# Performance work log

Measured on AMD Instinct MI355X. Metric: run time of the kernel, lower is better.

The kernel has to match this reference:

```python
import math
import jax, jax.numpy as jnp
import numpy as np

RATIO = 0.5
N_CHANNELS = 64
B = 64
N_PER = 8192  # nodes per batch element (equal counts for a regular reference)
D_POS = 3


def setup_inputs() -> dict:
    key = jax.random.key(0)
    k1, k2, k3 = jax.random.split(key, 3)
    N = B * N_PER
    positions = jax.random.normal(k1, (N, D_POS), dtype=jnp.float32)
    weights = jax.random.normal(k2, (N, N_CHANNELS), dtype=jnp.float32)
    w = jax.random.normal(k3, (N_CHANNELS,), dtype=jnp.float32)  # SelectTopK learnable vector
    batch = jnp.full((B,), N_PER, dtype=jnp.int32)  # per-batch-element node counts
    return {"positions": positions, "weights": weights, "w": w, "batch": batch}


def reference(positions, weights, w, batch):
    # SelectTopK: score = tanh((x @ w) / ||w||), then per-batch top-ceil(ratio*n) selection.
    n_b = batch.shape[0]
    n_per = positions.shape[0] // n_b
    k = int(math.ceil(RATIO * n_per))

    score = jnp.tanh((weights @ w) / jnp.linalg.norm(w))          # [N]
    top_vals, top_idx = jax.lax.top_k(score.reshape(n_b, n_per), k)  # [B,k] each

    # global node indices of selected nodes (descending score within each batch element)
    node_index = (top_idx + jnp.arange(n_b, dtype=top_idx.dtype)[:, None] * n_per).reshape(-1)  # [B*k]

    pos_sel = positions[node_index]                               # [B*k, D_POS]
    w_sel = weights[node_index] * top_vals.reshape(-1)[:, None]   # [B*k, C] gated by score
    # histc recount: each batch element keeps exactly k nodes
    new_batch = jnp.full((n_b,), k, dtype=jnp.int32)
    return pos_sel, w_sel, new_batch
```

## Files before the change

kernel.cpp:

```cpp
#include <hip/hip_runtime.h>
#include <math.h>

#define C 64
#define DPOS 3
#define NPER 8192
#define KK 4096

typedef unsigned long long ull;

__device__ __forceinline__ ull make_key(float s, unsigned idx) {
    unsigned u = __float_as_uint(s);
    unsigned o = (u >> 31) ? ~u : (u | 0x80000000u);
    unsigned d = ~o;
    return ((ull)d << 32) | (ull)idx;
}
__device__ __forceinline__ float key_score(ull key) {
    unsigned o = ~(unsigned)(key >> 32);
    unsigned u = (o >> 31) ? (o & 0x7FFFFFFFu) : ~o;
    return __uint_as_float(u);
}

__global__ __launch_bounds__(256) void score_kernel(const float* __restrict__ weights,
                                                    const float* __restrict__ w,
                                                    ull* __restrict__ keys, int n) {
    int wid = (blockIdx.x * blockDim.x + threadIdx.x) >> 6;
    int lane = threadIdx.x & 63;
    int c4 = lane & 15, sub = lane >> 4;
    const float4* wv4 = (const float4*)w;
    float nrm = 0.f;
    #pragma unroll
    for (int i = 0; i < 16; ++i) {
        float4 t = wv4[i];
        nrm += t.x * t.x + t.y * t.y + t.z * t.z + t.w * t.w;
    }
    float nw = sqrtf(nrm);
    float4 wv = wv4[c4];
    #pragma unroll
    for (int it = 0; it < 4; ++it) {
        int r = wid * 16 + it * 4 + sub;
        float4 x = ((const float4*)weights)[(size_t)r * 16 + c4];
        float acc = x.x * wv.x + x.y * wv.y + x.z * wv.z + x.w * wv.w;
        #pragma unroll
        for (int off = 8; off >= 1; off >>= 1) acc += __shfl_xor(acc, off, 16);
        if (c4 == 0 && r < n)
            keys[r] = make_key(tanhf(acc / nw), (unsigned)(r & (NPER - 1)));
    }
}

#define CH 2048
#define CTH 1024
__global__ __launch_bounds__(CTH) void sort_chunk(ull* __restrict__ keys) {
    __shared__ ull lds[CH];
    const int tid = threadIdx.x;
    ull* bk = keys + (size_t)blockIdx.x * CH;
    #pragma unroll
    for (int s = 0; s < CH / CTH; ++s) lds[tid + s * CTH] = bk[tid + s * CTH];
    for (unsigned k = 2; k <= CH; k <<= 1) {
        for (unsigned j = k >> 1; j > 0; j >>= 1) {
            __syncthreads();
            #pragma unroll
            for (int s = 0; s < CH / CTH; ++s) {
                unsigned i = tid + s * CTH;
                unsigned ixj = i ^ j;
                if (ixj > i) {
                    ull a = lds[i], b = lds[ixj];
                    bool up = ((i & k) == 0);
                    if ((a > b) == up) { lds[i] = b; lds[ixj] = a; }
                }
            }
        }
    }
    __syncthreads();
    #pragma unroll
    for (int s = 0; s < CH / CTH; ++s) bk[tid + s * CTH] = lds[tid + s * CTH];
}

#define MT 256
#define MTILE 1024
__global__ __launch_bounds__(MT) void merge_tiled(const ull* __restrict__ src,
                                                  ull* __restrict__ dst,
                                                  int L, int tilesPerPair, int outStride) {
    __shared__ ull in[MTILE];
    __shared__ ull ob[MTILE];
    __shared__ int sAB[2];
    int tile = blockIdx.x;
    int pair = tile / tilesPerPair;
    int o0 = (tile - pair * tilesPerPair) * MTILE;
    const ull* A = src + (size_t)pair * (2 * L);
    const ull* B = A + L;
    ull* D = dst + (size_t)pair * outStride;
    int tid = threadIdx.x;
    if (tid < 2) {
        int o = o0 + tid * MTILE;
        int lo = o - L; if (lo < 0) lo = 0;
        int hi = o < L ? o : L;
        while (lo < hi) {
            int m = (lo + hi) >> 1;
            if (A[m] < B[o - 1 - m]) lo = m + 1; else hi = m;
        }
        sAB[tid] = lo;
    }
    __syncthreads();
    int aLo = sAB[0], aHi = sAB[1];
    int na = aHi - aLo;
    int bLo = o0 - aLo;
    int nb2 = MTILE - na;
    for (int i = tid; i < na; i += MT) in[i] = A[aLo + i];
    for (int i = tid; i < nb2; i += MT) in[na + i] = B[bLo + i];
    __syncthreads();
    int o = tid * 4;
    int lo = o - nb2; if (lo < 0) lo = 0;
    int hi = o < na ? o : na;
    while (lo < hi) {
        int m = (lo + hi) >> 1;
        if (in[m] < in[na + o - 1 - m]) lo = m + 1; else hi = m;
    }
    int a = lo, b = o - lo;
    #pragma unroll
    for (int t = 0; t < 4; ++t) {
        bool fromA = (b >= nb2) || (a < na && in[a] < in[na + b]);
        ob[o + t] = fromA ? in[a++] : in[na + b++];
    }
    __syncthreads();
    for (int i = tid; i < MTILE; i += MT) D[o0 + i] = ob[i];
}

__global__ __launch_bounds__(1024) void sort_full(ull* __restrict__ keys) {
    __shared__ ull lds[NPER];
    const unsigned tid = threadIdx.x;
    ull* bk = keys + (size_t)blockIdx.x * NPER;
    #pragma unroll
    for (int s = 0; s < NPER / 1024; ++s) lds[tid + s * 1024] = bk[tid + s * 1024];
    for (unsigned k = 2; k <= NPER; k <<= 1) {
        for (unsigned j = k >> 1; j > 0; j >>= 1) {
            __syncthreads();
            #pragma unroll
            for (int s = 0; s < NPER / 1024; ++s) {
                unsigned i = tid + s * 1024;
                unsigned ixj = i ^ j;
                if (ixj > i) {
                    ull a = lds[i], b = lds[ixj];
                    bool up = ((i & k) == 0);
                    if ((a > b) == up) { lds[i] = b; lds[ixj] = a; }
                }
            }
        }
    }
    __syncthreads();
    #pragma unroll
    for (int s = 0; s < NPER / 1024; ++s) bk[tid + s * 1024] = lds[tid + s * 1024];
}

__global__ __launch_bounds__(256) void gather_kernel(const float* __restrict__ positions,
                                                     const float* __restrict__ weights,
                                                     const ull* __restrict__ keys,
                                                     float* __restrict__ out_pos,
                                                     float* __restrict__ out_w,
                                                     float* __restrict__ out_batch,
                                                     int rows, int nb, int kstr) {
    int gid = blockIdx.x * blockDim.x + threadIdx.x;
    if (gid < nb) out_batch[gid] = (float)KK;
    int lane = gid & 63;
    int sub = lane >> 4, c4 = lane & 15;
    int r = (gid >> 6) * 4 + sub;
    if (r >= rows) return;
    int b = r >> 12;
    int j = r & (KK - 1);
    ull key = keys[(size_t)b * kstr + j];
    unsigned idx = (unsigned)key;
    size_t node = ((size_t)b << 13) + idx;
    float s = key_score(key);
    float4 x = ((const float4*)weights)[node * 16 + c4];
    float4 y; y.x = x.x * s; y.y = x.y * s; y.z = x.z * s; y.w = x.w * s;
    ((float4*)out_w)[(size_t)r * 16 + c4] = y;
    if (c4 < DPOS)
        out_pos[(size_t)r * DPOS + c4] = positions[node * DPOS + c4];
}

extern "C" void kernel_launch(void* const* d_in, const int* in_sizes, int n_in,
                              void* d_out, int out_size, void* d_ws, size_t ws_size,
                              hipStream_t stream) {
    const float* positions = (const float*)d_in[0];
    const float* weights   = (const float*)d_in[1];
    const float* w         = (const float*)d_in[2];

    int n  = in_sizes[1] / C;
    int nb = in_sizes[3];
    int rows = nb * KK;

    ull* bufA = (ull*)d_ws;
    ull* bufB = bufA + n;
    bool have_dbuf = ws_size >= (size_t)n * 2 * sizeof(ull);

    score_kernel<<<n / 64, 256, 0, stream>>>(weights, w, bufA, n);

    const ull* sorted_keys;
    int kstr;
    if (have_dbuf) {
        sort_chunk<<<n / CH, CTH, 0, stream>>>(bufA);
        merge_tiled<<<n / MTILE, MT, 0, stream>>>(bufA, bufB, 2048, 4, 4096);
        merge_tiled<<<(nb * KK) / MTILE, MT, 0, stream>>>(bufB, bufA, 4096, 4, KK);
        sorted_keys = bufA; kstr = KK;
    } else {
        sort_full<<<nb, 1024, 0, stream>>>(bufA);
        sorted_keys = bufA; kstr = NPER;
    }

    long long gthreads = (long long)(rows / 4) * 64;
    gather_kernel<<<(int)((gthreads + 255) / 256), 256, 0, stream>>>(
        positions, weights, sorted_keys, (float*)d_out,
        (float*)d_out + (size_t)rows * DPOS,
        (float*)d_out + (size_t)rows * (DPOS + C),
        rows, nb, kstr);
}
```

Baseline: 280.5 us.

## Fuse scoring into chunk sort and merge each batch in one LDS kernel

The score computation now writes keys straight into shared memory inside the 2048-element bitonic chunk sort, so the key buffer no longer makes a separate global round trip. The two tiled global merge passes are replaced by one kernel per batch element. That kernel loads all 8192 sorted keys into LDS, runs the 2048→4096 merge in shared memory, and writes only the top 4096 from the final merge. This removes two launches and several global key read/write passes. The cost is much lower parallelism: the score pass now runs on only 256 large blocks, and the merge on one block per batch. That may hurt memory-level parallelism when streaming the weights.

```diff
diff --git a/kernel.cpp b/kernel.cpp
--- a/kernel.cpp
+++ b/kernel.cpp
@@ -20,12 +20,13 @@
     return __uint_as_float(u);
 }
 
-__global__ __launch_bounds__(256) void score_kernel(const float* __restrict__ weights,
-                                                    const float* __restrict__ w,
-                                                    ull* __restrict__ keys, int n) {
-    int wid = (blockIdx.x * blockDim.x + threadIdx.x) >> 6;
-    int lane = threadIdx.x & 63;
-    int c4 = lane & 15, sub = lane >> 4;
+#define CH 2048
+#define CTH 1024
+__global__ __launch_bounds__(CTH) void score_sort(const float* __restrict__ weights,
+                                                  const float* __restrict__ w,
+                                                  ull* __restrict__ keys) {
+    __shared__ ull lds[CH];
+    const int tid = threadIdx.x;
     const float4* wv4 = (const float4*)w;
     float nrm = 0.f;
     #pragma unroll
@@ -34,27 +35,20 @@
         nrm += t.x * t.x + t.y * t.y + t.z * t.z + t.w * t.w;
     }
     float nw = sqrtf(nrm);
+    const int r16 = tid >> 4;
+    const int c4  = tid & 15;
     float4 wv = wv4[c4];
-    #pragma unroll
-    for (int it = 0; it < 4; ++it) {
-        int r = wid * 16 + it * 4 + sub;
-        float4 x = ((const float4*)weights)[(size_t)r * 16 + c4];
+    const size_t base = (size_t)blockIdx.x * CH;
+    #pragma unroll 4
+    for (int it = 0; it < CH / 64; ++it) {
+        int rl = it * 64 + r16;
+        float4 x = ((const float4*)weights)[(base + rl) * 16 + c4];
         float acc = x.x * wv.x + x.y * wv.y + x.z * wv.z + x.w * wv.w;
         #pragma unroll
         for (int off = 8; off >= 1; off >>= 1) acc += __shfl_xor(acc, off, 16);
-        if (c4 == 0 && r < n)
-            keys[r] = make_key(tanhf(acc / nw), (unsigned)(r & (NPER - 1)));
-    }
-}
-
-#define CH 2048
-#define CTH 1024
-__global__ __launch_bounds__(CTH) void sort_chunk(ull* __restrict__ keys) {
-    __shared__ ull lds[CH];
-    const int tid = threadIdx.x;
-    ull* bk = keys + (size_t)blockIdx.x * CH;
-    #pragma unroll
-    for (int s = 0; s < CH / CTH; ++s) lds[tid + s * CTH] = bk[tid + s * CTH];
+        if (c4 == 0)
+            lds[rl] = make_key(tanhf(acc / nw), (unsigned)((base + rl) & (NPER - 1)));
+    }
     for (unsigned k = 2; k <= CH; k <<= 1) {
         for (unsigned j = k >> 1; j > 0; j >>= 1) {
             __syncthreads();
@@ -72,57 +66,58 @@
     }
     __syncthreads();
     #pragma unroll
-    for (int s = 0; s < CH / CTH; ++s) bk[tid + s * CTH] = lds[tid + s * CTH];
-}
-
-#define MT 256
-#define MTILE 1024
-__global__ __launch_bounds__(MT) void merge_tiled(const ull* __restrict__ src,
-                                                  ull* __restrict__ dst,
-                                                  int L, int tilesPerPair, int outStride) {
-    __shared__ ull in[MTILE];
-    __shared__ ull ob[MTILE];
-    __shared__ int sAB[2];
-    int tile = blockIdx.x;
-    int pair = tile / tilesPerPair;
-    int o0 = (tile - pair * tilesPerPair) * MTILE;
-    const ull* A = src + (size_t)pair * (2 * L);
-    const ull* B = A + L;
-    ull* D = dst + (size_t)pair * outStride;
-    int tid = threadIdx.x;
-    if (tid < 2) {
-        int o = o0 + tid * MTILE;
-        int lo = o - L; if (lo < 0) lo = 0;
-        int hi = o < L ? o : L;
+    for (int s = 0; s < CH / CTH; ++s) keys[base + tid + s * CTH] = lds[tid + s * CTH];
+}
+
+__global__ __launch_bounds__(1024) void merge_batch(const ull* __restrict__ src,
+                                                    ull* __restrict__ dst) {
+    __shared__ ull ld[NPER];
+    const int tid = threadIdx.x;
+    const ull* bk = src + (size_t)blockIdx.x * NPER;
+    #pragma unroll
+    for (int s = 0; s < NPER / 1024; ++s) ld[tid + s * 1024] = bk[tid + s * 1024];
+    __syncthreads();
+    ull r[8];
+    {
+        int p = tid >> 9;
+        int o = (tid & 511) * 8;
+        const ull* A = ld + p * 4096;
+        const ull* B = A + 2048;
+        int lo = o - 2048; if (lo < 0) lo = 0;
+        int hi = o < 2048 ? o : 2048;
         while (lo < hi) {
             int m = (lo + hi) >> 1;
             if (A[m] < B[o - 1 - m]) lo = m + 1; else hi = m;
         }
-        sAB[tid] = lo;
-    }
-    __syncthreads();
-    int aLo = sAB[0], aHi = sAB[1];
-    int na = aHi - aLo;
-    int bLo = o0 - aLo;
-    int nb2 = MTILE - na;
-    for (int i = tid; i < na; i += MT) in[i] = A[aLo + i];
-    for (int i = tid; i < nb2; i += MT) in[na + i] = B[bLo + i];
-    __syncthreads();
-    int o = tid * 4;
-    int lo = o - nb2; if (lo < 0) lo = 0;
-    int hi = o < na ? o : na;
-    while (lo < hi) {
-        int m = (lo + hi) >> 1;
-        if (in[m] < in[na + o - 1 - m]) lo = m + 1; else hi = m;
-    }
-    int a = lo, b = o - lo;
-    #pragma unroll
-    for (int t = 0; t < 4; ++t) {
-        bool fromA = (b >= nb2) || (a < na && in[a] < in[na + b]);
-        ob[o + t] = fromA ? in[a++] : in[na + b++];
-    }
-    __syncthreads();
-    for (int i = tid; i < MTILE; i += MT) D[o0 + i] = ob[i];
+        int a = lo, b = o - lo;
+        #pragma unroll
+        for (int t = 0; t < 8; ++t) {
+            bool fromA = (b >= 2048) || (a < 2048 && A[a] < B[b]);
+            r[t] = fromA ? A[a++] : B[b++];
+        }
+        __syncthreads();
+        #pragma unroll
+        for (int t = 0; t < 8; ++t) ld[p * 4096 + o + t] = r[t];
+        __syncthreads();
+    }
+    {
+        int o = tid * 4;
+        const ull* A = ld;
+        const ull* B = ld + 4096;
+        int lo = o - 4096; if (lo < 0) lo = 0;
+        int hi = o < 4096 ? o : 4096;
+        while (lo < hi) {
+            int m = (lo + hi) >> 1;
+            if (A[m] < B[o - 1 - m]) lo = m + 1; else hi = m;
+        }
+        int a = lo, b = o - lo;
+        ull* D = dst + (size_t)blockIdx.x * KK + o;
+        #pragma unroll
+        for (int t = 0; t < 4; ++t) {
+            bool fromA = (b >= 4096) || (a < 4096 && A[a] < B[b]);
+            D[t] = fromA ? A[a++] : B[b++];
+        }
+    }
 }
 
 __global__ __launch_bounds__(1024) void sort_full(ull* __restrict__ keys) {
@@ -190,17 +185,15 @@
 
     ull* bufA = (ull*)d_ws;
     ull* bufB = bufA + n;
-    bool have_dbuf = ws_size >= (size_t)n * 2 * sizeof(ull);
-
-    score_kernel<<<n / 64, 256, 0, stream>>>(weights, w, bufA, n);
+    bool have_dbuf = ws_size >= ((size_t)n + (size_t)rows) * sizeof(ull);
+
+    score_sort<<<n / CH, CTH, 0, stream>>>(weights, w, bufA);
 
     const ull* sorted_keys;
     int kstr;
     if (have_dbuf) {
-        sort_chunk<<<n / CH, CTH, 0, stream>>>(bufA);
-        merge_tiled<<<n / MTILE, MT, 0, stream>>>(bufA, bufB, 2048, 4, 4096);
-        merge_tiled<<<(nb * KK) / MTILE, MT, 0, stream>>>(bufB, bufA, 4096, 4, KK);
-        sorted_keys = bufA; kstr = KK;
+        merge_batch<<<nb, 1024, 0, stream>>>(bufA, bufB);
+        sorted_keys = bufB; kstr = KK;
     } else {
         sort_full<<<nb, 1024, 0, stream>>>(bufA);
         sorted_keys = bufA; kstr = NPER;
```

New measurement: 272.5 us. -2.9%, faster.
